# Kernel tuning notes

Hardware: AMD Instinct MI355X
Metric: run time of the kernel (lower is better)

Reference implementation:

```python
import jax, jax.numpy as jnp
import numpy as np

N_NODES = 50000


def setup_inputs() -> dict:
    key = jax.random.key(0)
    k_x, k_e, k_w1, k_w2 = jax.random.split(key, 4)
    in_c, hid, out_c = 256, 128, 64
    x = jax.random.normal(k_x, (N_NODES, in_c), dtype=jnp.float32)
    edge_index = jax.random.randint(k_e, (2, 800000), 0, N_NODES, dtype=jnp.int64)
    # Glorot-ish scaled weights (faithful to GCNConv default init scale)
    W1 = jax.random.normal(k_w1, (in_c, hid), dtype=jnp.float32) * (1.0 / np.sqrt(in_c))
    b1 = jnp.zeros((hid,), dtype=jnp.float32)
    W2 = jax.random.normal(k_w2, (hid, out_c), dtype=jnp.float32) * (1.0 / np.sqrt(hid))
    b2 = jnp.zeros((out_c,), dtype=jnp.float32)
    return {"x": x, "edge_index": edge_index, "W1": W1, "b1": b1, "W2": W2, "b2": b2}


def _gcn_norm(edge_index, n_nodes):
    # Add self loops, compute symmetric normalization D^-1/2 A D^-1/2.
    loop = jnp.arange(n_nodes, dtype=edge_index.dtype)
    src = jnp.concatenate([edge_index[0], loop])
    dst = jnp.concatenate([edge_index[1], loop])
    deg = jax.ops.segment_sum(jnp.ones_like(dst, dtype=jnp.float32), dst,
                              num_segments=n_nodes)
    dis = jnp.where(deg > 0, jax.lax.rsqrt(deg), 0.0)  # deg_inv_sqrt
    norm = dis[src] * dis[dst]  # [E + N]
    return src, dst, norm


def _gcn_conv(x, W, b, src, dst, norm, n_nodes):
    h = x @ W                                  # [N, F_out] dense transform first
    msgs = h[src] * norm[:, None]              # edge-wise gather + scale
    agg = jax.ops.segment_sum(msgs, dst, num_segments=n_nodes)  # scatter-add
    return agg + b


def reference(x, edge_index, W1, b1, W2, b2):
    n = x.shape[0]
    src, dst, norm = _gcn_norm(edge_index, n)  # cached=True: same norm both layers
    h = _gcn_conv(x, W1, b1, src, dst, norm, n)
    h = jax.nn.relu(h)
    # Dropout is identity in eval mode (deterministic reference)
    return _gcn_conv(h, W2, b2, src, dst, norm, n)
```

## Files before the change

### kernel.cpp

```cpp
#include <hip/hip_runtime.h>


#define IN_C 256
#define HID 128
#define OUTC 64
#define NBLK 128

typedef __attribute__((ext_vector_type(8))) short short8;
typedef __attribute__((ext_vector_type(4))) float f32x4;

__device__ __forceinline__ void bf16split(float f, ushort& h, ushort& l) {
    unsigned u = __float_as_uint(f);
    h = (ushort)(u >> 16);
    float hf = __uint_as_float(u & 0xFFFF0000u);
    unsigned v = __float_as_uint(f - hf);
    l = (ushort)((v + 0x7FFF + ((v >> 16) & 1)) >> 16);
}

__device__ __forceinline__ ushort f2bf(float f) {
    unsigned u = __float_as_uint(f);
    return (ushort)((u + 0x7FFF + ((u >> 16) & 1)) >> 16);
}
__device__ __forceinline__ float bf2f(ushort u) {
    return __uint_as_float((unsigned)u << 16);
}

__device__ __forceinline__ void* lds_addr(void* base, int row, int kelem) {
    int byte = row * 128 + kelem * 2;
    byte ^= (row & 7) << 4;
    return (char*)base + byte;
}

__device__ __forceinline__ int edge_at(const void* ei, long long idx, int is32) {
    return is32 ? ((const int*)ei)[idx] : (int)((const long long*)ei)[idx];
}

__global__ void detect_kernel(const unsigned long long* ei, int* flag) {
    if (threadIdx.x == 0 && blockIdx.x == 0) {
        int is32 = 0;
        for (int i = 0; i < 64; ++i)
            if (ei[i] >> 32) { is32 = 1; break; }
        *flag = is32;
    }
}

__global__ void wtrans_kernel(const float* __restrict__ W1, const float* __restrict__ W2,
                              ushort* __restrict__ w1h, ushort* __restrict__ w1l,
                              ushort* __restrict__ w2h, ushort* __restrict__ w2l) {
    int id = blockIdx.x * blockDim.x + threadIdx.x;
    if (id < HID * IN_C) {
        int n = id >> 8, k = id & 255;
        ushort h, l; bf16split(W1[k * HID + n], h, l);
        w1h[id] = h; w1l[id] = l;
    }
    if (id < OUTC * HID) {
        int n = id >> 7, k = id & 127;
        ushort h, l; bf16split(W2[k * OUTC + n], h, l);
        w2h[id] = h; w2l[id] = l;
    }
}

__global__ __launch_bounds__(256) void bin_count(const void* ei, const int* __restrict__ flag,
                                                 int* __restrict__ blkcnt, int E, int nb) {
    __shared__ int h[256];
    int t = threadIdx.x;
    h[t] = 0;
    __syncthreads();
    int is32 = *flag;
    int chunk = (E + gridDim.x - 1) / gridDim.x;
    long long s0 = (long long)blockIdx.x * chunk;
    long long s1 = s0 + chunk; if (s1 > E) s1 = E;
    for (long long e = s0 + t; e < s1; e += 256) {
        int d = edge_at(ei, (long long)E + e, is32);
        atomicAdd(&h[d >> 8], 1);
    }
    __syncthreads();
    if (t < nb) blkcnt[t * NBLK + blockIdx.x] = h[t];
}

__global__ __launch_bounds__(256) void bin_scan(int* __restrict__ blkcnt,
                                                int* __restrict__ bbase, int nb) {
    __shared__ int sh[256];
    int t = threadIdx.x;
    int tot = 0;
    if (t < nb) {
        int4* p = (int4*)&blkcnt[t * NBLK];
        int run = 0;
        for (int i = 0; i < NBLK / 4; ++i) {
            int4 v = p[i]; int4 o;
            o.x = run; run += v.x; o.y = run; run += v.y;
            o.z = run; run += v.z; o.w = run; run += v.w;
            p[i] = o;
        }
        tot = run;
    }
    sh[t] = tot;
    __syncthreads();
    for (int d = 1; d < 256; d <<= 1) {
        int add = (t >= d) ? sh[t - d] : 0;
        __syncthreads();
        sh[t] += add;
        __syncthreads();
    }
    if (t < nb) {
        bbase[t] = sh[t] - tot;
        if (t == nb - 1) bbase[nb] = sh[t];
    }
}

__global__ __launch_bounds__(256) void bin_scatter(const void* ei, const int* __restrict__ flag,
                                                   const int* __restrict__ blkcnt,
                                                   const int* __restrict__ bbase,
                                                   unsigned* __restrict__ coarse, int E, int nb) {
    __shared__ int cur[256];
    int t = threadIdx.x;
    if (t < nb) cur[t] = bbase[t] + blkcnt[t * NBLK + blockIdx.x];
    __syncthreads();
    int is32 = *flag;
    int chunk = (E + gridDim.x - 1) / gridDim.x;
    long long s0 = (long long)blockIdx.x * chunk;
    long long s1 = s0 + chunk; if (s1 > E) s1 = E;
    for (long long e = s0 + t; e < s1; e += 256) {
        int s = edge_at(ei, e, is32);
        int d = edge_at(ei, (long long)E + e, is32);
        int p = atomicAdd(&cur[d >> 8], 1);
        coarse[p] = (unsigned)s | ((unsigned)(d & 255) << 17);
    }
}

__global__ __launch_bounds__(256) void fine_kernel(const unsigned* __restrict__ coarse,
                                                   const int* __restrict__ bbase,
                                                   int* __restrict__ row_ptr,
                                                   float* __restrict__ dis,
                                                   int* __restrict__ epk, int N, int nb) {
    __shared__ int h[256], cur[256], sh[256];
    int b = blockIdx.x, t = threadIdx.x;
    int nb0 = b << 8;
    int e0b = bbase[b], e1b = bbase[b + 1];
    h[t] = 0;
    __syncthreads();
    for (int e = e0b + t; e < e1b; e += 256)
        atomicAdd(&h[(coarse[e] >> 17) & 0xFF], 1);
    __syncthreads();
    int cnt = h[t];
    sh[t] = cnt;
    __syncthreads();
    for (int d = 1; d < 256; d <<= 1) {
        int add = (t >= d) ? sh[t - d] : 0;
        __syncthreads();
        sh[t] += add;
        __syncthreads();
    }
    int excl = sh[t] - cnt;
    int node = nb0 + t;
    if (node < N) {
        row_ptr[node] = e0b + excl;
        dis[node] = rsqrtf((float)cnt + 1.0f);
        if (node == N - 1) row_ptr[N] = e0b + sh[t];
    }
    cur[t] = e0b + excl;
    __syncthreads();
    for (int e = e0b + t; e < e1b; e += 256) {
        unsigned r = coarse[e];
        int p = atomicAdd(&cur[(r >> 17) & 0xFF], 1);
        epk[p] = (int)(r & 0x1FFFF);
    }
}

__global__ void zsent_kernel(ushort* a, ushort* b, ushort* c) {
    int t = threadIdx.x;
    if (t < 64) { a[t] = 0; b[t] = 0; c[t] = 0; }
}

__global__ __launch_bounds__(256) void gemm1_mfma(const float* __restrict__ X,
                                                  const ushort* __restrict__ WTh,
                                                  const ushort* __restrict__ WTl,
                                                  const float* __restrict__ dis,
                                                  ushort* __restrict__ HB, int N) {
    __shared__ ushort XH[64 * 64], XL[64 * 64];
    __shared__ ushort WH[128 * 64], WL[128 * 64];
    int t = threadIdx.x;
    int lane = t & 63, w = t >> 6;
    int m_off = (w >> 1) * 32, n_off = (w & 1) * 64;
    long long row0 = (long long)blockIdx.x * 64;
    size_t sstride = (size_t)(N + 1) * 64;
    f32x4 acc[2][4] = {};
    for (int k0 = 0; k0 < IN_C; k0 += 64) {
        __syncthreads();
        {
            int xr = t >> 4, xc = (t & 15) * 4;
            #pragma unroll
            for (int p = 0; p < 4; ++p) {
                int row = xr + p * 16;
                long long gr = row0 + row;
                float4 v = make_float4(0.f, 0.f, 0.f, 0.f);
                if (gr < N) v = *(const float4*)&X[gr * IN_C + k0 + xc];
                ushort4 h4, l4;
                bf16split(v.x, h4.x, l4.x); bf16split(v.y, h4.y, l4.y);
                bf16split(v.z, h4.z, l4.z); bf16split(v.w, h4.w, l4.w);
                *(ushort4*)lds_addr(XH, row, xc) = h4;
                *(ushort4*)lds_addr(XL, row, xc) = l4;
            }
        }
        {
            int wn = t >> 3, wk = (t & 7) * 8;
            #pragma unroll
            for (int p = 0; p < 4; ++p) {
                int n = wn + p * 32;
                *(short8*)lds_addr(WH, n, wk) = *(const short8*)&WTh[n * IN_C + k0 + wk];
                *(short8*)lds_addr(WL, n, wk) = *(const short8*)&WTl[n * IN_C + k0 + wk];
            }
        }
        __syncthreads();
        #pragma unroll
        for (int kk = 0; kk < 2; ++kk) {
            int ke = kk * 32 + (lane >> 4) * 8;
            short8 ah[2], al[2], bh[4], bl[4];
            #pragma unroll
            for (int mi = 0; mi < 2; ++mi) {
                int r = m_off + mi * 16 + (lane & 15);
                ah[mi] = *(short8*)lds_addr(XH, r, ke);
                al[mi] = *(short8*)lds_addr(XL, r, ke);
            }
            #pragma unroll
            for (int ni = 0; ni < 4; ++ni) {
                int r = n_off + ni * 16 + (lane & 15);
                bh[ni] = *(short8*)lds_addr(WH, r, ke);
                bl[ni] = *(short8*)lds_addr(WL, r, ke);
            }
            #pragma unroll
            for (int mi = 0; mi < 2; ++mi)
                #pragma unroll
                for (int ni = 0; ni < 4; ++ni) {
                    acc[mi][ni] = __builtin_amdgcn_mfma_f32_16x16x32_bf16(ah[mi], bh[ni], acc[mi][ni], 0, 0, 0);
                    acc[mi][ni] = __builtin_amdgcn_mfma_f32_16x16x32_bf16(ah[mi], bl[ni], acc[mi][ni], 0, 0, 0);
                    acc[mi][ni] = __builtin_amdgcn_mfma_f32_16x16x32_bf16(al[mi], bh[ni], acc[mi][ni], 0, 0, 0);
                }
        }
    }
    int cr = (lane >> 4) * 4, cc = lane & 15;
    #pragma unroll
    for (int mi = 0; mi < 2; ++mi)
        #pragma unroll
        for (int j = 0; j < 4; ++j) {
            long long gr = row0 + m_off + mi * 16 + cr + j;
            if (gr < N) {
                float dv = dis[gr];
                #pragma unroll
                for (int ni = 0; ni < 4; ++ni) {
                    int col = n_off + ni * 16 + cc;
                    HB[(size_t)(col >> 6) * sstride + gr * 64 + (col & 63)] =
                        f2bf(acc[mi][ni][j] * dv);
                }
            }
        }
}

__global__ __launch_bounds__(256) void gemm2_mfma(const float* __restrict__ A,
                                                  const float* __restrict__ b1,
                                                  const ushort* __restrict__ WTh,
                                                  const ushort* __restrict__ WTl,
                                                  const float* __restrict__ dis,
                                                  ushort* __restrict__ HB, int N) {
    __shared__ ushort AH[64 * 64], AL[64 * 64];
    __shared__ ushort WH[64 * 64], WL[64 * 64];
    int t = threadIdx.x;
    int lane = t & 63, w = t >> 6;
    int m_off = (w >> 1) * 32, n_off = (w & 1) * 32;
    long long row0 = (long long)blockIdx.x * 64;
    f32x4 acc[2][2] = {};
    for (int k0 = 0; k0 < HID; k0 += 64) {
        __syncthreads();
        {
            int xr = t >> 4, xc = (t & 15) * 4;
            float4 bb = *(const float4*)&b1[k0 + xc];
            #pragma unroll
            for (int p = 0; p < 4; ++p) {
                int row = xr + p * 16;
                long long gr = row0 + row;
                float4 v = make_float4(0.f, 0.f, 0.f, 0.f);
                if (gr < N) {
                    v = *(const float4*)&A[gr * HID + k0 + xc];
                    v.x = fmaxf(v.x + bb.x, 0.f); v.y = fmaxf(v.y + bb.y, 0.f);
                    v.z = fmaxf(v.z + bb.z, 0.f); v.w = fmaxf(v.w + bb.w, 0.f);
                }
                ushort4 h4, l4;
                bf16split(v.x, h4.x, l4.x); bf16split(v.y, h4.y, l4.y);
                bf16split(v.z, h4.z, l4.z); bf16split(v.w, h4.w, l4.w);
                *(ushort4*)lds_addr(AH, row, xc) = h4;
                *(ushort4*)lds_addr(AL, row, xc) = l4;
            }
        }
        {
            int wn = t >> 3, wk = (t & 7) * 8;
            #pragma unroll
            for (int p = 0; p < 2; ++p) {
                int n = wn + p * 32;
                *(short8*)lds_addr(WH, n, wk) = *(const short8*)&WTh[n * HID + k0 + wk];
                *(short8*)lds_addr(WL, n, wk) = *(const short8*)&WTl[n * HID + k0 + wk];
            }
        }
        __syncthreads();
        #pragma unroll
        for (int kk = 0; kk < 2; ++kk) {
            int ke = kk * 32 + (lane >> 4) * 8;
            short8 ah[2], al[2], bh[2], bl[2];
            #pragma unroll
            for (int mi = 0; mi < 2; ++mi) {
                int r = m_off + mi * 16 + (lane & 15);
                ah[mi] = *(short8*)lds_addr(AH, r, ke);
                al[mi] = *(short8*)lds_addr(AL, r, ke);
            }
            #pragma unroll
            for (int ni = 0; ni < 2; ++ni) {
                int r = n_off + ni * 16 + (lane & 15);
                bh[ni] = *(short8*)lds_addr(WH, r, ke);
                bl[ni] = *(short8*)lds_addr(WL, r, ke);
            }
            #pragma unroll
            for (int mi = 0; mi < 2; ++mi)
                #pragma unroll
                for (int ni = 0; ni < 2; ++ni) {
                    acc[mi][ni] = __builtin_amdgcn_mfma_f32_16x16x32_bf16(ah[mi], bh[ni], acc[mi][ni], 0, 0, 0);
                    acc[mi][ni] = __builtin_amdgcn_mfma_f32_16x16x32_bf16(ah[mi], bl[ni], acc[mi][ni], 0, 0, 0);
                    acc[mi][ni] = __builtin_amdgcn_mfma_f32_16x16x32_bf16(al[mi], bh[ni], acc[mi][ni], 0, 0, 0);
                }
        }
    }
    int cr = (lane >> 4) * 4, cc = lane & 15;
    #pragma unroll
    for (int mi = 0; mi < 2; ++mi)
        #pragma unroll
        for (int j = 0; j < 4; ++j) {
            long long gr = row0 + m_off + mi * 16 + cr + j;
            if (gr < N) {
                float dv = dis[gr];
                #pragma unroll
                for (int ni = 0; ni < 2; ++ni)
                    HB[gr * OUTC + n_off + ni * 16 + cc] = f2bf(acc[mi][ni][j] * dv);
            }
        }
}

__global__ __launch_bounds__(256) void seg_agg_v5(const ushort* __restrict__ Hsl,
                                                  const float* __restrict__ dis,
                                                  const int* __restrict__ row_ptr,
                                                  const int* __restrict__ epk,
                                                  const float* __restrict__ bias,
                                                  float* __restrict__ out,
                                                  int N, int ostride) {
    int lane = threadIdx.x & 63;
    int node = (int)(((long long)blockIdx.x * blockDim.x + threadIdx.x) >> 6);
    if (node >= N) return;
    const ushort* hl = Hsl + lane;
    float acc = bf2f(hl[node * 64]);
    int e0 = row_ptr[node], e1 = row_ptr[node + 1];
    for (int base = e0; base < e1; base += 64) {
        int cnt = min(64, e1 - base);
        int rec = epk[min(base + lane, e1 - 1)];
        for (int u0 = 0; u0 < cnt; u0 += 16) {
            float hv[16];
            #pragma unroll
            for (int u = 0; u < 16; ++u) {
                int s = (u0 + u < cnt) ? __builtin_amdgcn_readlane(rec, u0 + u) : N;
                hv[u] = bf2f(hl[s * 64]);
            }
            #pragma unroll
            for (int u = 0; u < 16; ++u)
                acc += hv[u];
        }
    }
    float r = dis[node] * acc;
    if (bias) r += bias[lane];
    out[(size_t)node * ostride + lane] = r;
}

extern "C" void kernel_launch(void* const* d_in, const int* in_sizes, int n_in,
                              void* d_out, int out_size, void* d_ws, size_t ws_size,
                              hipStream_t stream) {
    const float* x  = (const float*)d_in[0];
    const void*  ei = d_in[1];
    const float* W1 = (const float*)d_in[2];
    const float* b1 = (const float*)d_in[3];
    const float* W2 = (const float*)d_in[4];
    const float* b2 = (const float*)d_in[5];
    float* out = (float*)d_out;
    int N = in_sizes[0] / IN_C;
    int E = in_sizes[1] / 2;
    int nb = (N + 255) >> 8;

    char* ws = (char*)d_ws;
    size_t off = 0;
    auto alloc = [&](size_t bytes) {
        void* p = ws + off;
        off += ((bytes + 255) / 256) * 256;
        return p;
    };
    int*      flag    = (int*)alloc(4);
    int*      blkcnt  = (int*)alloc((size_t)nb * NBLK * 4);
    int*      bbase   = (int*)alloc(((size_t)nb + 1) * 4);
    int*      row_ptr = (int*)alloc(((size_t)N + 1) * 4);
    float*    dis     = (float*)alloc((size_t)N * 4);
    unsigned* coarse  = (unsigned*)alloc((size_t)E * 4);
    int*      epk     = (int*)alloc((size_t)E * 4);
    ushort*   w1h     = (ushort*)alloc((size_t)HID * IN_C * 2);
    ushort*   w1l     = (ushort*)alloc((size_t)HID * IN_C * 2);
    ushort*   w2h     = (ushort*)alloc((size_t)OUTC * HID * 2);
    ushort*   w2l     = (ushort*)alloc((size_t)OUTC * HID * 2);
    size_t sstride    = (size_t)(N + 1) * 64;
    ushort*   H1b     = (ushort*)alloc(2 * sstride * 2);
    float*    AG1     = (float*)alloc((size_t)N * HID * 4);
    ushort*   H2b     = (ushort*)alloc(sstride * 2);

    detect_kernel<<<1, 64, 0, stream>>>((const unsigned long long*)ei, flag);
    wtrans_kernel<<<(HID * IN_C + 255) / 256, 256, 0, stream>>>(W1, W2, w1h, w1l, w2h, w2l);
    bin_count<<<NBLK, 256, 0, stream>>>(ei, flag, blkcnt, E, nb);
    bin_scan<<<1, 256, 0, stream>>>(blkcnt, bbase, nb);
    bin_scatter<<<NBLK, 256, 0, stream>>>(ei, flag, blkcnt, bbase, coarse, E, nb);
    fine_kernel<<<nb, 256, 0, stream>>>(coarse, bbase, row_ptr, dis, epk, N, nb);
    zsent_kernel<<<1, 64, 0, stream>>>(H1b + (size_t)N * 64,
                                       H1b + sstride + (size_t)N * 64,
                                       H2b + (size_t)N * 64);
    gemm1_mfma<<<(N + 63) / 64, 256, 0, stream>>>(x, w1h, w1l, dis, H1b, N);

    int agg_blocks = (int)(((long long)N * 64 + 255) / 256);
    seg_agg_v5<<<agg_blocks, 256, 0, stream>>>(H1b,           dis, row_ptr, epk,
                                               nullptr, AG1,      N, HID);
    seg_agg_v5<<<agg_blocks, 256, 0, stream>>>(H1b + sstride, dis, row_ptr, epk,
                                               nullptr, AG1 + 64, N, HID);
    gemm2_mfma<<<(N + 63) / 64, 256, 0, stream>>>(AG1, b1, w2h, w2l, dis, H2b, N);
    seg_agg_v5<<<agg_blocks, 256, 0, stream>>>(H2b, dis, row_ptr, epk,
                                               b2, out, N, OUTC);
}
```

Measured before the change: 166.8 us.

## Load GEMM operands directly from global memory into MFMA registers, dropping LDS staging

Both dense GEMM kernels stop staging X/A and weight tiles through swizzled shared memory. Each lane now loads its own MFMA fragment straight from global memory and does the bf16 hi/lo split (plus bias and ReLU for layer 2) in registers. This removes the LDS writes and reads and the two barriers per K step. In exchange, X and W are re-read redundantly across waves (X by the two column waves, W by every block through L2), and the fragment loads are less coalesced. Out-of-range rows are clamped to the last row instead of zero-filled, which is safe because those results are masked at store time.

After: 200.6 us. 20.3% more time.

```diff
diff --git a/kernel.cpp b/kernel.cpp
--- a/kernel.cpp
+++ b/kernel.cpp
@@ -17,18 +17,20 @@
     l = (ushort)((v + 0x7FFF + ((v >> 16) & 1)) >> 16);
 }
 
+__device__ __forceinline__ void split8(const float* p, short8& h8, short8& l8) {
+    #pragma unroll
+    for (int i = 0; i < 8; ++i) {
+        ushort h, l; bf16split(p[i], h, l);
+        h8[i] = (short)h; l8[i] = (short)l;
+    }
+}
+
 __device__ __forceinline__ ushort f2bf(float f) {
     unsigned u = __float_as_uint(f);
     return (ushort)((u + 0x7FFF + ((u >> 16) & 1)) >> 16);
 }
 __device__ __forceinline__ float bf2f(ushort u) {
     return __uint_as_float((unsigned)u << 16);
-}
-
-__device__ __forceinline__ void* lds_addr(void* base, int row, int kelem) {
-    int byte = row * 128 + kelem * 2;
-    byte ^= (row & 7) << 4;
-    return (char*)base + byte;
 }
 
 __device__ __forceinline__ int edge_at(const void* ei, long long idx, int is32) {
@@ -177,56 +179,35 @@
                                                   const ushort* __restrict__ WTl,
                                                   const float* __restrict__ dis,
                                                   ushort* __restrict__ HB, int N) {
-    __shared__ ushort XH[64 * 64], XL[64 * 64];
-    __shared__ ushort WH[128 * 64], WL[128 * 64];
     int t = threadIdx.x;
     int lane = t & 63, w = t >> 6;
     int m_off = (w >> 1) * 32, n_off = (w & 1) * 64;
     long long row0 = (long long)blockIdx.x * 64;
     size_t sstride = (size_t)(N + 1) * 64;
     f32x4 acc[2][4] = {};
+    long long ar[2];
+    #pragma unroll
+    for (int mi = 0; mi < 2; ++mi) {
+        long long gr = row0 + m_off + mi * 16 + (lane & 15);
+        ar[mi] = (gr < N ? gr : (long long)(N - 1)) * IN_C;
+    }
     for (int k0 = 0; k0 < IN_C; k0 += 64) {
-        __syncthreads();
-        {
-            int xr = t >> 4, xc = (t & 15) * 4;
-            #pragma unroll
-            for (int p = 0; p < 4; ++p) {
-                int row = xr + p * 16;
-                long long gr = row0 + row;
-                float4 v = make_float4(0.f, 0.f, 0.f, 0.f);
-                if (gr < N) v = *(const float4*)&X[gr * IN_C + k0 + xc];
-                ushort4 h4, l4;
-                bf16split(v.x, h4.x, l4.x); bf16split(v.y, h4.y, l4.y);
-                bf16split(v.z, h4.z, l4.z); bf16split(v.w, h4.w, l4.w);
-                *(ushort4*)lds_addr(XH, row, xc) = h4;
-                *(ushort4*)lds_addr(XL, row, xc) = l4;
-            }
-        }
-        {
-            int wn = t >> 3, wk = (t & 7) * 8;
-            #pragma unroll
-            for (int p = 0; p < 4; ++p) {
-                int n = wn + p * 32;
-                *(short8*)lds_addr(WH, n, wk) = *(const short8*)&WTh[n * IN_C + k0 + wk];
-                *(short8*)lds_addr(WL, n, wk) = *(const short8*)&WTl[n * IN_C + k0 + wk];
-            }
-        }
-        __syncthreads();
         #pragma unroll
         for (int kk = 0; kk < 2; ++kk) {
-            int ke = kk * 32 + (lane >> 4) * 8;
+            int ke = k0 + kk * 32 + (lane >> 4) * 8;
             short8 ah[2], al[2], bh[4], bl[4];
             #pragma unroll
             for (int mi = 0; mi < 2; ++mi) {
-                int r = m_off + mi * 16 + (lane & 15);
-                ah[mi] = *(short8*)lds_addr(XH, r, ke);
-                al[mi] = *(short8*)lds_addr(XL, r, ke);
+                float xv[8];
+                *(float4*)&xv[0] = *(const float4*)&X[ar[mi] + ke];
+                *(float4*)&xv[4] = *(const float4*)&X[ar[mi] + ke + 4];
+                split8(xv, ah[mi], al[mi]);
             }
             #pragma unroll
             for (int ni = 0; ni < 4; ++ni) {
-                int r = n_off + ni * 16 + (lane & 15);
-                bh[ni] = *(short8*)lds_addr(WH, r, ke);
-                bl[ni] = *(short8*)lds_addr(WL, r, ke);
+                int n = n_off + ni * 16 + (lane & 15);
+                bh[ni] = *(const short8*)&WTh[n * IN_C + ke];
+                bl[ni] = *(const short8*)&WTl[n * IN_C + ke];
             }
             #pragma unroll
             for (int mi = 0; mi < 2; ++mi)
@@ -262,60 +243,39 @@
                                                   const ushort* __restrict__ WTl,
                                                   const float* __restrict__ dis,
                                                   ushort* __restrict__ HB, int N) {
-    __shared__ ushort AH[64 * 64], AL[64 * 64];
-    __shared__ ushort WH[64 * 64], WL[64 * 64];
     int t = threadIdx.x;
     int lane = t & 63, w = t >> 6;
     int m_off = (w >> 1) * 32, n_off = (w & 1) * 32;
     long long row0 = (long long)blockIdx.x * 64;
     f32x4 acc[2][2] = {};
+    long long ar[2];
+    #pragma unroll
+    for (int mi = 0; mi < 2; ++mi) {
+        long long gr = row0 + m_off + mi * 16 + (lane & 15);
+        ar[mi] = (gr < N ? gr : (long long)(N - 1)) * HID;
+    }
     for (int k0 = 0; k0 < HID; k0 += 64) {
-        __syncthreads();
-        {
-            int xr = t >> 4, xc = (t & 15) * 4;
-            float4 bb = *(const float4*)&b1[k0 + xc];
-            #pragma unroll
-            for (int p = 0; p < 4; ++p) {
-                int row = xr + p * 16;
-                long long gr = row0 + row;
-                float4 v = make_float4(0.f, 0.f, 0.f, 0.f);
-                if (gr < N) {
-                    v = *(const float4*)&A[gr * HID + k0 + xc];
-                    v.x = fmaxf(v.x + bb.x, 0.f); v.y = fmaxf(v.y + bb.y, 0.f);
-                    v.z = fmaxf(v.z + bb.z, 0.f); v.w = fmaxf(v.w + bb.w, 0.f);
-                }
-                ushort4 h4, l4;
-                bf16split(v.x, h4.x, l4.x); bf16split(v.y, h4.y, l4.y);
-                bf16split(v.z, h4.z, l4.z); bf16split(v.w, h4.w, l4.w);
-                *(ushort4*)lds_addr(AH, row, xc) = h4;
-                *(ushort4*)lds_addr(AL, row, xc) = l4;
-            }
-        }
-        {
-            int wn = t >> 3, wk = (t & 7) * 8;
-            #pragma unroll
-            for (int p = 0; p < 2; ++p) {
-                int n = wn + p * 32;
-                *(short8*)lds_addr(WH, n, wk) = *(const short8*)&WTh[n * HID + k0 + wk];
-                *(short8*)lds_addr(WL, n, wk) = *(const short8*)&WTl[n * HID + k0 + wk];
-            }
-        }
-        __syncthreads();
         #pragma unroll
         for (int kk = 0; kk < 2; ++kk) {
-            int ke = kk * 32 + (lane >> 4) * 8;
+            int ke = k0 + kk * 32 + (lane >> 4) * 8;
+            float bv[8];
+            *(float4*)&bv[0] = *(const float4*)&b1[ke];
+            *(float4*)&bv[4] = *(const float4*)&b1[ke + 4];
             short8 ah[2], al[2], bh[2], bl[2];
             #pragma unroll
             for (int mi = 0; mi < 2; ++mi) {
-                int r = m_off + mi * 16 + (lane & 15);
-                ah[mi] = *(short8*)lds_addr(AH, r, ke);
-                al[mi] = *(short8*)lds_addr(AL, r, ke);
+                float av[8];
+                *(float4*)&av[0] = *(const float4*)&A[ar[mi] + ke];
+                *(float4*)&av[4] = *(const float4*)&A[ar[mi] + ke + 4];
+                #pragma unroll
+                for (int i = 0; i < 8; ++i) av[i] = fmaxf(av[i] + bv[i], 0.f);
+                split8(av, ah[mi], al[mi]);
             }
             #pragma unroll
             for (int ni = 0; ni < 2; ++ni) {
-                int r = n_off + ni * 16 + (lane & 15);
-                bh[ni] = *(short8*)lds_addr(WH, r, ke);
-                bl[ni] = *(short8*)lds_addr(WL, r, ke);
+                int n = n_off + ni * 16 + (lane & 15);
+                bh[ni] = *(const short8*)&WTh[n * HID + ke];
+                bl[ni] = *(const short8*)&WTl[n * HID + ke];
             }
             #pragma unroll
             for (int mi = 0; mi < 2; ++mi)
```
